# Kernel optimization log

Measured on AMD Instinct MI355X. Metric: run time of the kernel, lower is better.

Reference implementation:

```python
import jax, jax.numpy as jnp
import numpy as np

# Dimensions: N sites, B batch, D bond dim, d physical dim, C output classes
N, B, D, d, C = 1024, 256, 16, 2, 10
STDDEV = 1e-5
INIT_DIAG = 1.0


def setup_inputs() -> dict:
    key = jax.random.key(0)
    k1, k2, k3 = jax.random.split(key, 3)
    x = jax.random.normal(k1, (N, B, d), dtype=jnp.float32)
    eye = jnp.eye(D, dtype=jnp.float32)
    # tensor[n,:,:,i] = init_diag * I + stddev * noise  (matches TF init)
    tensor = INIT_DIAG * eye[None, :, :, None] + STDDEV * jax.random.normal(k2, (N, D, D, d), dtype=jnp.float32)
    # Aout[c] = I + stddev * noise
    Aout = eye[None, :, :] + STDDEV * jax.random.normal(k3, (C, D, D), dtype=jnp.float32)
    return {"x": x, "tensor": tensor, "Aout": Aout}


def _chain_prod(A):
    # A: (n, b, D, D) -> ordered matrix-chain product (b, D, D), log-depth tree.
    # Faithful to parallel_contract: pairwise einsum per level; odd leftover is
    # kept at the end of the list (order-preserving, associativity-equivalent).
    while A.shape[0] > 1:
        n = A.shape[0]
        half = n // 2
        prod = jnp.einsum('nblk,nbkr->nblr', A[0:2 * half:2], A[1:2 * half:2])
        if n % 2 == 1:
            prod = jnp.concatenate([prod, A[-1:]], axis=0)
        A = prod
    return A[0]


def reference(x, tensor, Aout):
    # A: (N, B, D, D) site matrices after contracting input features
    A = jnp.einsum('nbi,nlri->nblr', x, tensor)
    nhalf = A.shape[0] // 2
    # Left half product, take row 0 (left boundary); right half, take col 0
    Al = _chain_prod(A[:nhalf])[:, 0, :]   # (B, D)
    Ar = _chain_prod(A[nhalf:])[:, :, 0]   # (B, D)
    # out[b,o] = Al[b] @ Aout[o] @ Ar[b]
    return jnp.einsum('bl,olr,br->bo', Al, Aout, Ar)
```

## Files before the change

kernel.cpp:

```cpp
#include <hip/hip_runtime.h>


#define BATCH  256
#define NCLS   10
#define NSITES 1024
#define NGRP   16
#define SEGLEN 16

typedef __attribute__((ext_vector_type(8))) short short8;
typedef __attribute__((ext_vector_type(4))) float f32x4;
typedef __attribute__((ext_vector_type(4))) unsigned short us4;

static __device__ __forceinline__ unsigned short bf16tr(float f) {
    return (unsigned short)(__builtin_bit_cast(unsigned, f) >> 16);
}
static __device__ __forceinline__ unsigned short bf16rne(float f) {
    unsigned u = __builtin_bit_cast(unsigned, f);
    u += 0x7FFFu + ((u >> 16) & 1u);
    return (unsigned short)(u >> 16);
}
static __device__ __forceinline__ float bf16tof(unsigned short h) {
    return __builtin_bit_cast(float, (unsigned)h << 16);
}

__global__ __launch_bounds__(256) void ta_pack_kernel(
    const float* __restrict__ tensor, unsigned short* __restrict__ Ta)
{
    __shared__ float s[512];
    const int n = blockIdx.x, t = threadIdx.x;
    *(float2*)(s + 2 * t) = *(const float2*)(tensor + (size_t)n * 512 + 2 * t);
    __syncthreads();
    const int o0 = 2 * t, m = o0 >> 5, k0 = o0 & 31;
    const float v0 = s[(k0 & 15) * 32 + m * 2 + (k0 >> 4)];
    const int k1 = k0 + 1;
    const float v1 = s[(k1 & 15) * 32 + m * 2 + (k1 >> 4)];
    const unsigned pk = (unsigned)bf16rne(v0) | ((unsigned)bf16rne(v1) << 16);
    ((unsigned*)Ta)[(size_t)n * 256 + t] = pk;
}

__global__ __launch_bounds__(256) void chain_kernel(
    const float* __restrict__ x,
    const unsigned short* __restrict__ Ta,
    unsigned short* __restrict__ M2)
{
    __shared__ unsigned short rm[4 * 256];
    __shared__ unsigned short cm[4 * 256];
    const int t = threadIdx.x, wave = t >> 6, lane = t & 63;
    const int quad = lane >> 4, l15 = lane & 15;
    const int b = blockIdx.x >> 4, g = blockIdx.x & 15;
    const int seg = g * 4 + wave, n0 = seg * SEGLEN;

    const int qm = quad & 1;
    const int bidx0 = (32 * qm + l15) * 4;
    const int bidx1 = bidx0 + 64;

    f32x4 d;
#pragma unroll
    for (int r = 0; r < 4; ++r) d[r] = (quad * 4 + r == l15) ? 1.0f : 0.0f;

    const float2* __restrict__ xp = (const float2*)x;

#pragma unroll 4
    for (int s = 0; s < SEGLEN; ++s) {
        const int n = n0 + s;
        const float2 xv = xp[(size_t)n * BATCH + b];
        const float xs = (quad < 2) ? xv.x : xv.y;
        const short8 af = *(const short8*)(Ta + (size_t)n * 512 + l15 * 32 + quad * 8);
        float w[8];
#pragma unroll
        for (int r = 0; r < 4; ++r) {
            w[r]     = __builtin_bit_cast(float,
                        __builtin_amdgcn_ds_bpermute(bidx0, __builtin_bit_cast(int, d[r])));
            w[4 + r] = __builtin_bit_cast(float,
                        __builtin_amdgcn_ds_bpermute(bidx1, __builtin_bit_cast(int, d[r])));
        }
        short8 bf;
#pragma unroll
        for (int j = 0; j < 8; ++j) bf[j] = (short)bf16tr(xs * w[j]);
        f32x4 c = {0.0f, 0.0f, 0.0f, 0.0f};
        d = __builtin_amdgcn_mfma_f32_16x16x32_bf16(af, bf, c, 0, 0, 0);
    }

#pragma unroll
    for (int r = 0; r < 4; ++r)
        rm[wave * 256 + (quad * 4 + r) * 16 + l15] = bf16tr(d[r]);
    {
        us4 pk = {bf16tr(d[0]), bf16tr(d[1]), bf16tr(d[2]), bf16tr(d[3])};
        *(us4*)(cm + wave * 256 + l15 * 16 + quad * 4) = pk;
    }
    __syncthreads();

    const short8 z8 = {0, 0, 0, 0, 0, 0, 0, 0};

    short8 af1 = z8, bf1 = z8;
    if (wave < 2 && quad < 2) {
        af1 = *(const short8*)(rm + (2 * wave + 1) * 256 + l15 * 16 + quad * 8);
        bf1 = *(const short8*)(cm + (2 * wave) * 256 + l15 * 16 + quad * 8);
    }
    __syncthreads();
    if (wave < 2) {
        f32x4 c = {0.0f, 0.0f, 0.0f, 0.0f};
        f32x4 q = __builtin_amdgcn_mfma_f32_16x16x32_bf16(af1, bf1, c, 0, 0, 0);
#pragma unroll
        for (int r = 0; r < 4; ++r)
            rm[wave * 256 + (quad * 4 + r) * 16 + l15] = bf16tr(q[r]);
        us4 pk = {bf16tr(q[0]), bf16tr(q[1]), bf16tr(q[2]), bf16tr(q[3])};
        *(us4*)(cm + wave * 256 + l15 * 16 + quad * 4) = pk;
    }
    __syncthreads();

    if (wave == 0) {
        short8 af2 = z8, bf2 = z8;
        if (quad < 2) {
            af2 = *(const short8*)(rm + 1 * 256 + l15 * 16 + quad * 8);
            bf2 = *(const short8*)(cm + 0 * 256 + l15 * 16 + quad * 8);
        }
        f32x4 c = {0.0f, 0.0f, 0.0f, 0.0f};
        f32x4 rr = __builtin_amdgcn_mfma_f32_16x16x32_bf16(af2, bf2, c, 0, 0, 0);
        us4 pk = {bf16tr(rr[0]), bf16tr(rr[1]), bf16tr(rr[2]), bf16tr(rr[3])};
        *(us4*)(M2 + ((size_t)b * NGRP + g) * 256 + l15 * 16 + quad * 4) = pk;
    }
}

__global__ __launch_bounds__(256) void combine_kernel(
    const unsigned short* __restrict__ M2,
    const float* __restrict__ Aout,
    float* __restrict__ out)
{
    __shared__ unsigned short rm[16 * 256];
    __shared__ unsigned short cm[16 * 256];
    const int b = blockIdx.x, t = threadIdx.x;
    const int wave = t >> 6, lane = t & 63, quad = lane >> 4, l15 = lane & 15;

    const short8* __restrict__ src = (const short8*)(M2 + (size_t)b * NGRP * 256);
#pragma unroll
    for (int i2 = 0; i2 < 2; ++i2) {
        const int i = t + 256 * i2;
        const short8 v = src[i];
        *((short8*)cm + i) = v;
        const int mat = i >> 5, c = (i >> 1) & 15, r0 = (i & 1) * 8;
#pragma unroll
        for (int e = 0; e < 8; ++e)
            rm[mat * 256 + (r0 + e) * 16 + c] = (unsigned short)v[e];
    }
    __syncthreads();

    const short8 z8 = {0, 0, 0, 0, 0, 0, 0, 0};

    for (int lvl = 0; lvl < 3; ++lvl) {
        const int np = 8 >> lvl;
        short8 afr[2], bfr[2];
        int pids[2], nmine = 0;
        for (int p = wave; p < np; p += 4) {
            short8 a = z8, bb = z8;
            if (quad < 2) {
                a  = *(const short8*)(rm + (2 * p + 1) * 256 + l15 * 16 + quad * 8);
                bb = *(const short8*)(cm + (2 * p) * 256 + l15 * 16 + quad * 8);
            }
            afr[nmine] = a; bfr[nmine] = bb; pids[nmine] = p; ++nmine;
        }
        __syncthreads();
        for (int ii = 0; ii < nmine; ++ii) {
            f32x4 c = {0.0f, 0.0f, 0.0f, 0.0f};
            f32x4 r = __builtin_amdgcn_mfma_f32_16x16x32_bf16(afr[ii], bfr[ii], c, 0, 0, 0);
            const int p = pids[ii];
#pragma unroll
            for (int rr = 0; rr < 4; ++rr)
                rm[p * 256 + (quad * 4 + rr) * 16 + l15] = bf16tr(r[rr]);
            us4 pk = {bf16tr(r[0]), bf16tr(r[1]), bf16tr(r[2]), bf16tr(r[3])};
            *(us4*)(cm + p * 256 + l15 * 16 + quad * 4) = pk;
        }
        __syncthreads();
    }

    if (t < NCLS * 16) {
        const int o = t >> 4, r = t & 15;
        const float vr = bf16tof(rm[256 + r]);
        float s = 0.0f;
#pragma unroll
        for (int l = 0; l < 16; ++l)
            s = __builtin_fmaf(bf16tof(rm[l * 16]), Aout[((size_t)o * 16 + l) * 16 + r], s);
        s *= vr;
#pragma unroll
        for (int off = 8; off > 0; off >>= 1)
            s += __shfl_xor(s, off, 16);
        if (r == 0) out[(size_t)b * NCLS + o] = s;
    }
}

extern "C" void kernel_launch(void* const* d_in, const int* in_sizes, int n_in,
                              void* d_out, int out_size, void* d_ws, size_t ws_size,
                              hipStream_t stream)
{
    const float* x      = (const float*)d_in[0];
    const float* tensor = (const float*)d_in[1];
    const float* Aout   = (const float*)d_in[2];
    float* out = (float*)d_out;

    unsigned short* Ta = (unsigned short*)d_ws;
    unsigned short* M2 = (unsigned short*)((char*)d_ws + (1 << 20));

    ta_pack_kernel<<<NSITES, 256, 0, stream>>>(tensor, Ta);
    chain_kernel<<<BATCH * NGRP, 256, 0, stream>>>(x, Ta, M2);
    combine_kernel<<<BATCH, 256, 0, stream>>>(M2, Aout, out);
}
```

Before: 90.38 us.

## Use 16x16x16 MFMA with operand-side input contraction, dropping cross-lane permutes

The chain step now contracts the physical index into the site matrix operand (two FMAs per element, with both physical slices packed in the Ta layout), so the running product feeds MFMA directly as the B operand. This removes the per-step ds_bpermute shuffles and the zero-padded 16x16x32 MFMA in favour of a dense 16x16x16 bf16 MFMA. Ta is repacked to match the new fragment layout, and the block-to-(batch, group) mapping is swapped so that neighbouring blocks share site data. It adds FMA work per step, and packing by truncation rather than round-to-nearest may change numerics slightly.

```diff
diff --git a/kernel.cpp b/kernel.cpp
--- a/kernel.cpp
+++ b/kernel.cpp
@@ -7,8 +7,10 @@
 #define NGRP   16
 #define SEGLEN 16
 
-typedef __attribute__((ext_vector_type(8))) short short8;
 typedef __attribute__((ext_vector_type(4))) float f32x4;
+typedef __attribute__((ext_vector_type(4))) short short4b;
+typedef __attribute__((ext_vector_type(2))) unsigned uint2v;
+typedef __attribute__((ext_vector_type(4))) unsigned uint4v;
 typedef __attribute__((ext_vector_type(4))) unsigned short us4;
 
 static __device__ __forceinline__ unsigned short bf16tr(float f) {
@@ -22,6 +24,32 @@
 static __device__ __forceinline__ float bf16tof(unsigned short h) {
     return __builtin_bit_cast(float, (unsigned)h << 16);
 }
+static __device__ __forceinline__ unsigned fbits(float f) {
+    return __builtin_bit_cast(unsigned, f);
+}
+static __device__ __forceinline__ float lo16(unsigned u) {
+    return __builtin_bit_cast(float, u << 16);
+}
+static __device__ __forceinline__ float hi16(unsigned u) {
+    return __builtin_bit_cast(float, u & 0xffff0000u);
+}
+static __device__ __forceinline__ unsigned pkhi(float hi, float lo) {
+    return __builtin_amdgcn_perm(fbits(hi), fbits(lo), 0x07060302u);
+}
+static __device__ __forceinline__ short4b mk4(unsigned lo, unsigned hi) {
+    uint2v u; u.x = lo; u.y = hi;
+    return __builtin_bit_cast(short4b, u);
+}
+static __device__ __forceinline__ f32x4 mfma16(short4b a, short4b b, f32x4 c) {
+#if __has_builtin(__builtin_amdgcn_mfma_f32_16x16x16bf16_1k)
+    return __builtin_amdgcn_mfma_f32_16x16x16bf16_1k(a, b, c, 0, 0, 0);
+#else
+    f32x4 d;
+    asm volatile("v_mfma_f32_16x16x16_bf16 %0, %1, %2, %3"
+                 : "=v"(d) : "v"(a), "v"(b), "v"(c));
+    return d;
+#endif
+}
 
 __global__ __launch_bounds__(256) void ta_pack_kernel(
     const float* __restrict__ tensor, unsigned short* __restrict__ Ta)
@@ -30,12 +58,15 @@
     const int n = blockIdx.x, t = threadIdx.x;
     *(float2*)(s + 2 * t) = *(const float2*)(tensor + (size_t)n * 512 + 2 * t);
     __syncthreads();
-    const int o0 = 2 * t, m = o0 >> 5, k0 = o0 & 31;
-    const float v0 = s[(k0 & 15) * 32 + m * 2 + (k0 >> 4)];
-    const int k1 = k0 + 1;
-    const float v1 = s[(k1 & 15) * 32 + m * 2 + (k1 >> 4)];
-    const unsigned pk = (unsigned)bf16rne(v0) | ((unsigned)bf16rne(v1) << 16);
-    ((unsigned*)Ta)[(size_t)n * 256 + t] = pk;
+    const int o0 = 2 * t;
+    const int lane = o0 >> 3, e0 = o0 & 7;
+    const int q = lane >> 4, m = lane & 15;
+    const int i = e0 >> 2, j0 = e0 & 3;
+    const int k0 = 4 * q + j0;
+    const float v0 = s[k0 * 32 + m * 2 + i];
+    const float v1 = s[(k0 + 1) * 32 + m * 2 + i];
+    ((unsigned*)Ta)[(size_t)n * 256 + t] =
+        (unsigned)bf16rne(v0) | ((unsigned)bf16rne(v1) << 16);
 }
 
 __global__ __launch_bounds__(256) void chain_kernel(
@@ -43,42 +74,33 @@
     const unsigned short* __restrict__ Ta,
     unsigned short* __restrict__ M2)
 {
-    __shared__ unsigned short rm[4 * 256];
-    __shared__ unsigned short cm[4 * 256];
+    __shared__ __align__(16) unsigned short rm[4 * 256];
+    __shared__ __align__(16) unsigned short cm[4 * 256];
     const int t = threadIdx.x, wave = t >> 6, lane = t & 63;
     const int quad = lane >> 4, l15 = lane & 15;
-    const int b = blockIdx.x >> 4, g = blockIdx.x & 15;
+    const int b = blockIdx.x & 255, g = blockIdx.x >> 8;
     const int seg = g * 4 + wave, n0 = seg * SEGLEN;
 
-    const int qm = quad & 1;
-    const int bidx0 = (32 * qm + l15) * 4;
-    const int bidx1 = bidx0 + 64;
-
     f32x4 d;
 #pragma unroll
     for (int r = 0; r < 4; ++r) d[r] = (quad * 4 + r == l15) ? 1.0f : 0.0f;
 
     const float2* __restrict__ xp = (const float2*)x;
+    const uint4v* __restrict__ tp = (const uint4v*)Ta + (size_t)n0 * 64 + lane;
 
 #pragma unroll 4
     for (int s = 0; s < SEGLEN; ++s) {
         const int n = n0 + s;
         const float2 xv = xp[(size_t)n * BATCH + b];
-        const float xs = (quad < 2) ? xv.x : xv.y;
-        const short8 af = *(const short8*)(Ta + (size_t)n * 512 + l15 * 32 + quad * 8);
-        float w[8];
-#pragma unroll
-        for (int r = 0; r < 4; ++r) {
-            w[r]     = __builtin_bit_cast(float,
-                        __builtin_amdgcn_ds_bpermute(bidx0, __builtin_bit_cast(int, d[r])));
-            w[4 + r] = __builtin_bit_cast(float,
-                        __builtin_amdgcn_ds_bpermute(bidx1, __builtin_bit_cast(int, d[r])));
-        }
-        short8 bf;
-#pragma unroll
-        for (int j = 0; j < 8; ++j) bf[j] = (short)bf16tr(xs * w[j]);
-        f32x4 c = {0.0f, 0.0f, 0.0f, 0.0f};
-        d = __builtin_amdgcn_mfma_f32_16x16x32_bf16(af, bf, c, 0, 0, 0);
+        const uint4v tw = tp[(size_t)s * 64];
+        const float a0 = __builtin_fmaf(xv.x, lo16(tw.x), xv.y * lo16(tw.z));
+        const float a1 = __builtin_fmaf(xv.x, hi16(tw.x), xv.y * hi16(tw.z));
+        const float a2 = __builtin_fmaf(xv.x, lo16(tw.y), xv.y * lo16(tw.w));
+        const float a3 = __builtin_fmaf(xv.x, hi16(tw.y), xv.y * hi16(tw.w));
+        const short4b af = mk4(pkhi(a1, a0), pkhi(a3, a2));
+        const short4b bf = mk4(pkhi(d[1], d[0]), pkhi(d[3], d[2]));
+        f32x4 c0 = {0.0f, 0.0f, 0.0f, 0.0f};
+        d = mfma16(af, bf, c0);
     }
 
 #pragma unroll
@@ -90,17 +112,17 @@
     }
     __syncthreads();
 
-    const short8 z8 = {0, 0, 0, 0, 0, 0, 0, 0};
-
-    short8 af1 = z8, bf1 = z8;
-    if (wave < 2 && quad < 2) {
-        af1 = *(const short8*)(rm + (2 * wave + 1) * 256 + l15 * 16 + quad * 8);
-        bf1 = *(const short8*)(cm + (2 * wave) * 256 + l15 * 16 + quad * 8);
-    }
-    __syncthreads();
+    short4b af1 = {0, 0, 0, 0}, bf1 = {0, 0, 0, 0};
     if (wave < 2) {
-        f32x4 c = {0.0f, 0.0f, 0.0f, 0.0f};
-        f32x4 q = __builtin_amdgcn_mfma_f32_16x16x32_bf16(af1, bf1, c, 0, 0, 0);
+        af1 = __builtin_bit_cast(short4b,
+              *(const uint2v*)(rm + (2 * wave + 1) * 256 + l15 * 16 + quad * 4));
+        bf1 = __builtin_bit_cast(short4b,
+              *(const uint2v*)(cm + (2 * wave) * 256 + l15 * 16 + quad * 4));
+    }
+    __syncthreads();
+    if (wave < 2) {
+        f32x4 c0 = {0.0f, 0.0f, 0.0f, 0.0f};
+        f32x4 q = mfma16(af1, bf1, c0);
 #pragma unroll
         for (int r = 0; r < 4; ++r)
             rm[wave * 256 + (quad * 4 + r) * 16 + l15] = bf16tr(q[r]);
@@ -110,13 +132,12 @@
     __syncthreads();
 
     if (wave == 0) {
-        short8 af2 = z8, bf2 = z8;
-        if (quad < 2) {
-            af2 = *(const short8*)(rm + 1 * 256 + l15 * 16 + quad * 8);
-            bf2 = *(const short8*)(cm + 0 * 256 + l15 * 16 + quad * 8);
-        }
-        f32x4 c = {0.0f, 0.0f, 0.0f, 0.0f};
-        f32x4 rr = __builtin_amdgcn_mfma_f32_16x16x32_bf16(af2, bf2, c, 0, 0, 0);
+        const short4b af2 = __builtin_bit_cast(short4b,
+              *(const uint2v*)(rm + 1 * 256 + l15 * 16 + quad * 4));
+        const short4b bf2 = __builtin_bit_cast(short4b,
+              *(const uint2v*)(cm + 0 * 256 + l15 * 16 + quad * 4));
+        f32x4 c0 = {0.0f, 0.0f, 0.0f, 0.0f};
+        f32x4 rr = mfma16(af2, bf2, c0);
         us4 pk = {bf16tr(rr[0]), bf16tr(rr[1]), bf16tr(rr[2]), bf16tr(rr[3])};
         *(us4*)(M2 + ((size_t)b * NGRP + g) * 256 + l15 * 16 + quad * 4) = pk;
     }
@@ -127,10 +148,11 @@
     const float* __restrict__ Aout,
     float* __restrict__ out)
 {
-    __shared__ unsigned short rm[16 * 256];
-    __shared__ unsigned short cm[16 * 256];
+    __shared__ __align__(16) unsigned short rm[16 * 256];
+    __shared__ __align__(16) unsigned short cm[16 * 256];
     const int b = blockIdx.x, t = threadIdx.x;
     const int wave = t >> 6, lane = t & 63, quad = lane >> 4, l15 = lane & 15;
+    typedef __attribute__((ext_vector_type(8))) short short8;
 
     const short8* __restrict__ src = (const short8*)(M2 + (size_t)b * NGRP * 256);
 #pragma unroll
@@ -145,24 +167,21 @@
     }
     __syncthreads();
 
-    const short8 z8 = {0, 0, 0, 0, 0, 0, 0, 0};
-
     for (int lvl = 0; lvl < 3; ++lvl) {
         const int np = 8 >> lvl;
-        short8 afr[2], bfr[2];
+        short4b afr[2], bfr[2];
         int pids[2], nmine = 0;
         for (int p = wave; p < np; p += 4) {
-            short8 a = z8, bb = z8;
-            if (quad < 2) {
-                a  = *(const short8*)(rm + (2 * p + 1) * 256 + l15 * 16 + quad * 8);
-                bb = *(const short8*)(cm + (2 * p) * 256 + l15 * 16 + quad * 8);
-            }
-            afr[nmine] = a; bfr[nmine] = bb; pids[nmine] = p; ++nmine;
+            afr[nmine] = __builtin_bit_cast(short4b,
+                 *(const uint2v*)(rm + (2 * p + 1) * 256 + l15 * 16 + quad * 4));
+            bfr[nmine] = __builtin_bit_cast(short4b,
+                 *(const uint2v*)(cm + (2 * p) * 256 + l15 * 16 + quad * 4));
+            pids[nmine] = p; ++nmine;
         }
         __syncthreads();
         for (int ii = 0; ii < nmine; ++ii) {
-            f32x4 c = {0.0f, 0.0f, 0.0f, 0.0f};
-            f32x4 r = __builtin_amdgcn_mfma_f32_16x16x32_bf16(afr[ii], bfr[ii], c, 0, 0, 0);
+            f32x4 c0 = {0.0f, 0.0f, 0.0f, 0.0f};
+            f32x4 r = mfma16(afr[ii], bfr[ii], c0);
             const int p = pids[ii];
 #pragma unroll
             for (int rr = 0; rr < 4; ++rr)
```

New measurement: 81.53 us. 9.8% less time.
